# Kernel optimization log

Hardware: AMD Instinct MI355X
Metric: run time of the kernel (lower is better)

Reference implementation:

```python
import jax, jax.numpy as jnp
import numpy as np
from jax import lax

PRE_NMS_TOPN = 2000
POST_NMS_TOPN = 1000
NMS_THRESH = 0.7
MIN_BOX_SIZE = 4.0
BBOX_XFORM_CLIP = 4.135  # log(1000/16), standard clamp on dw/dh


def setup_inputs() -> dict:
    key = jax.random.key(0)
    k1, k2, k3, k4 = jax.random.split(key, 4)
    B, N = 8, 250000
    H, W = 800, 1333
    rpn_bbox_pred = jax.random.normal(k1, (B, N, 4), jnp.float32) * 0.5
    objectness = jax.random.normal(k2, (B, N), jnp.float32)
    # realistic anchors: centers inside image, sizes in [16, 256]
    ctr = jax.random.uniform(k3, (N, 2), jnp.float32) * jnp.array([W, H], jnp.float32)
    wh = jax.random.uniform(k4, (N, 2), jnp.float32) * 240.0 + 16.0
    anchors = jnp.concatenate([ctr - 0.5 * wh, ctr + 0.5 * wh], axis=-1)
    return {"rpn_bbox_pred": rpn_bbox_pred, "objectness": objectness,
            "anchors": anchors, "height": H, "width": W}


def _decode_clip(anchors, deltas, height, width):
    # anchors (1,N,4) broadcast against deltas (B,N,4); boxes are x1,y1,x2,y2
    aw = anchors[..., 2] - anchors[..., 0]
    ah = anchors[..., 3] - anchors[..., 1]
    ax = anchors[..., 0] + 0.5 * aw
    ay = anchors[..., 1] + 0.5 * ah
    dx, dy = deltas[..., 0], deltas[..., 1]
    dw = jnp.minimum(deltas[..., 2], BBOX_XFORM_CLIP)
    dh = jnp.minimum(deltas[..., 3], BBOX_XFORM_CLIP)
    px = dx * aw + ax
    py = dy * ah + ay
    pw = jnp.exp(dw) * aw
    ph = jnp.exp(dh) * ah
    x1 = jnp.clip(px - 0.5 * pw, 0.0, float(width))
    y1 = jnp.clip(py - 0.5 * ph, 0.0, float(height))
    x2 = jnp.clip(px + 0.5 * pw, 0.0, float(width))
    y2 = jnp.clip(py + 0.5 * ph, 0.0, float(height))
    return jnp.stack([x1, y1, x2, y2], axis=-1)


def _pairwise_iou(boxes):
    # boxes (K,4) -> iou (K,K)
    x1, y1, x2, y2 = boxes[:, 0], boxes[:, 1], boxes[:, 2], boxes[:, 3]
    area = (x2 - x1) * (y2 - y1)
    iw = jnp.maximum(jnp.minimum(x2[:, None], x2[None, :]) - jnp.maximum(x1[:, None], x1[None, :]), 0.0)
    ih = jnp.maximum(jnp.minimum(y2[:, None], y2[None, :]) - jnp.maximum(y1[:, None], y1[None, :]), 0.0)
    inter = iw * ih
    return inter / (area[:, None] + area[None, :] - inter + 1e-9)


def _nms_keep(boxes, valid):
    # sequential greedy NMS over score-sorted boxes (K,4); returns keep mask (K,)
    iou = lax.stop_gradient(_pairwise_iou(boxes))
    idxs = jnp.arange(PRE_NMS_TOPN)
    def body(i, keep):
        sup = (iou[i] > NMS_THRESH) & keep[i] & (idxs > i)
        return keep & (~sup)
    return lax.fori_loop(0, PRE_NMS_TOPN, body, valid)


def _per_image(boxes, scores):
    # boxes (N,4), scores (N,)
    ws = boxes[:, 2] - boxes[:, 0]
    hs = boxes[:, 3] - boxes[:, 1]
    size_ok = (ws >= MIN_BOX_SIZE) & (hs >= MIN_BOX_SIZE)
    masked = jnp.where(size_ok, scores, -jnp.inf)
    top_s, order = lax.top_k(masked, PRE_NMS_TOPN)   # descending sort + pre-NMS topN
    top_boxes = boxes[order]                          # (PRE,4)
    valid = top_s > -jnp.inf                          # boxes surviving size filter
    keep = _nms_keep(top_boxes, valid)
    # take first POST_NMS_TOPN kept boxes in score order (fixed-shape padding)
    sel = jnp.sort(jnp.where(keep, jnp.arange(PRE_NMS_TOPN), PRE_NMS_TOPN))[:POST_NMS_TOPN]
    out_valid = sel < PRE_NMS_TOPN
    sel_c = jnp.minimum(sel, PRE_NMS_TOPN - 1)
    out = jnp.where(out_valid[:, None], top_boxes[sel_c], 0.0)
    return out, out_valid


def reference(rpn_bbox_pred, objectness, anchors, height, width):
    proposals = _decode_clip(anchors[None], rpn_bbox_pred, height, width)  # (B,N,4)
    out, valid = jax.vmap(_per_image)(proposals, objectness)
    # padded equivalent of the ragged per-image list: (B,POST,4) boxes + (B,POST) validity
    return out, valid
```

## Files before the change

### kernel.cpp

```cpp
#include <hip/hip_runtime.h>
#include <hip/hip_bf16.h>

#define NBUCK 8192
#define P1B   64
#define CAP   4096
#define TOPN  2000
#define NP2   2048
#define OUTN  1000
#define NST   64
#define NSLOT 8
#define SLOTW 2048

typedef unsigned int u32x4 __attribute__((ext_vector_type(4)));
typedef __attribute__((address_space(1))) const unsigned GUP;
typedef __attribute__((address_space(3))) unsigned LUP;

__device__ __forceinline__ float4 decode_box(const float4 a, const float4 d, float W, float H) {
    float aw = a.z - a.x;
    float ah = a.w - a.y;
    float ax = a.x + 0.5f * aw;
    float ay = a.y + 0.5f * ah;
    float dw = fminf(d.z, 4.135f);
    float dh = fminf(d.w, 4.135f);
    float px = d.x * aw + ax;
    float py = d.y * ah + ay;
    float pw = expf(dw) * aw;
    float ph = expf(dh) * ah;
    float4 r;
    r.x = fminf(fmaxf(px - 0.5f * pw, 0.0f), W);
    r.y = fminf(fmaxf(py - 0.5f * ph, 0.0f), H);
    r.z = fminf(fmaxf(px + 0.5f * pw, 0.0f), W);
    r.w = fminf(fmaxf(py + 0.5f * ph, 0.0f), H);
    return r;
}

__device__ __forceinline__ unsigned score_key(const float4 a, const float4 d, float W, float H, float s) {
    float4 b = decode_box(a, d, W, H);
    bool ok = ((b.z - b.x) >= 4.0f) && ((b.w - b.y) >= 4.0f);
    float ms = ok ? s : -INFINITY;
    unsigned u = __float_as_uint(ms);
    return (u & 0x80000000u) ? ~u : (u | 0x80000000u);
}

__global__ void __launch_bounds__(1024) k_pass1(const float* __restrict__ pred,
        const float* __restrict__ obj, const float* __restrict__ anch,
        const int* __restrict__ Hp, const int* __restrict__ Wp,
        unsigned* __restrict__ keys, unsigned short* __restrict__ bhist,
        unsigned* __restrict__ cnt, unsigned* __restrict__ remInit, int N) {
    __shared__ unsigned h[NBUCK];
    int t = threadIdx.x;
    int b = blockIdx.y, g = blockIdx.x;
    if (g == 0 && t < 64) { if (t == 0) cnt[b * 64] = 0; remInit[b * 64 + t] = 0; }
    for (int i = t; i < NBUCK; i += 1024) h[i] = 0;
    __syncthreads();
    int chunk = (N + P1B - 1) / P1B;
    int base = g * chunk;
    int end = base + chunk; if (end > N) end = N;
    float W = (float)*Wp, H = (float)*Hp;
    for (int n = base + t; n < end; n += 1024) {
        float4 a = ((const float4*)anch)[n];
        float4 d = ((const float4*)pred)[(size_t)b * N + n];
        float s = obj[(size_t)b * N + n];
        unsigned key = score_key(a, d, W, H, s);
        keys[(size_t)b * N + n] = key;
        atomicAdd(&h[key >> 19], 1u);
    }
    __syncthreads();
    unsigned short* bh = bhist + ((size_t)(b * P1B + g)) * NBUCK;
    int i0 = t * 8;
    uint4 pk;
    pk.x = (h[i0 + 0] & 0xFFFFu) | (h[i0 + 1] << 16);
    pk.y = (h[i0 + 2] & 0xFFFFu) | (h[i0 + 3] << 16);
    pk.z = (h[i0 + 4] & 0xFFFFu) | (h[i0 + 5] << 16);
    pk.w = (h[i0 + 6] & 0xFFFFu) | (h[i0 + 7] << 16);
    *(uint4*)(bh + i0) = pk;
}

__global__ void __launch_bounds__(1024) k_scanA(const unsigned short* __restrict__ bhist,
                                                unsigned* __restrict__ hist32) {
    int b = blockIdx.y, p = blockIdx.x, t = threadIdx.x;
    int bkt = p * 1024 + t;
    const unsigned short* src = bhist + (size_t)b * P1B * NBUCK + bkt;
    unsigned acc = 0;
    #pragma unroll 8
    for (int g = 0; g < P1B; g++) acc += src[(size_t)g * NBUCK];
    hist32[b * NBUCK + bkt] = acc;
}

__global__ void k_scanB(const unsigned* __restrict__ hist32, unsigned* __restrict__ Lb) {
    __shared__ unsigned h[NBUCK];
    __shared__ unsigned csum[256];
    __shared__ unsigned suf[256];
    __shared__ int tcS;
    __shared__ unsigned befS;
    int b = blockIdx.x, t = threadIdx.x;
    const unsigned* src = hist32 + (size_t)b * NBUCK;
    for (int i = t * 4; i < NBUCK; i += 1024) {
        uint4 v = *(const uint4*)(src + i);
        h[i] = v.x; h[i + 1] = v.y; h[i + 2] = v.z; h[i + 3] = v.w;
    }
    if (t == 0) tcS = -1;
    __syncthreads();
    unsigned s = 0;
    for (int j = 0; j < 32; j++) s += h[t * 32 + j];
    csum[t] = s; suf[t] = s;
    __syncthreads();
    for (int d = 1; d < 256; d <<= 1) {
        unsigned v = (t + d < 256) ? suf[t + d] : 0;
        __syncthreads();
        suf[t] += v;
        __syncthreads();
    }
    if (suf[t] >= (unsigned)TOPN && (t == 255 || suf[t + 1] < (unsigned)TOPN)) {
        tcS = t; befS = (t == 255) ? 0u : suf[t + 1];
    }
    __syncthreads();
    if (t == 0) {
        unsigned L = 0;
        int tc = tcS;
        if (tc >= 0) {
            unsigned r = befS;
            for (int bkt = tc * 32 + 31;; bkt--) {
                r += h[bkt];
                if (r >= (unsigned)TOPN || bkt == tc * 32) { L = (unsigned)bkt; break; }
            }
        }
        Lb[b] = L;
    }
}

__global__ void k_collect(const unsigned* __restrict__ keys, const unsigned* __restrict__ Lb,
                          unsigned* __restrict__ count, unsigned long long* __restrict__ cand,
                          int N) {
    __shared__ unsigned lk[1024], ln[1024];
    __shared__ unsigned lcnt, lbase;
    int b = blockIdx.y, t = threadIdx.x;
    if (t == 0) lcnt = 0;
    __syncthreads();
    unsigned L = Lb[b];
    const unsigned* kb = keys + (size_t)b * N;
    int e = blockIdx.x * 256 + t;
    int n0 = e * 4;
    if (n0 + 3 < N) {
        uint4 kv = ((const uint4*)kb)[e];
        if ((kv.x >> 19) >= L) { unsigned p = atomicAdd(&lcnt, 1u); lk[p] = kv.x; ln[p] = n0; }
        if ((kv.y >> 19) >= L) { unsigned p = atomicAdd(&lcnt, 1u); lk[p] = kv.y; ln[p] = n0 + 1; }
        if ((kv.z >> 19) >= L) { unsigned p = atomicAdd(&lcnt, 1u); lk[p] = kv.z; ln[p] = n0 + 2; }
        if ((kv.w >> 19) >= L) { unsigned p = atomicAdd(&lcnt, 1u); lk[p] = kv.w; ln[p] = n0 + 3; }
    } else {
        for (int j = 0; j < 4; j++) {
            int n = n0 + j;
            if (n < N) {
                unsigned k = kb[n];
                if ((k >> 19) >= L) { unsigned p = atomicAdd(&lcnt, 1u); lk[p] = k; ln[p] = n; }
            }
        }
    }
    __syncthreads();
    if (t == 0) lbase = atomicAdd(&count[b * 64], lcnt);
    __syncthreads();
    unsigned c = lcnt, bs = lbase;
    for (unsigned i = t; i < c; i += 256) {
        unsigned pos = bs + i;
        if (pos < CAP) cand[(size_t)b * CAP + pos] =
            ((unsigned long long)lk[i] << 32) | (unsigned)(~ln[i]);
    }
}

#define REGX(e, p, d, lo)  ((lo) == (d) ? ((e) >= (p) ? (e) : (p)) : ((e) >= (p) ? (p) : (e)))

__global__ void __launch_bounds__(256) k_sort1(unsigned long long* __restrict__ cand,
        const unsigned* __restrict__ count) {
    __shared__ unsigned long long s[512];
    int b = blockIdx.x >> 3, g = blockIdx.x & 7;
    int t = threadIdx.x;
    unsigned cnt = count[b * 64]; if (cnt > CAP) cnt = CAP;
    unsigned long long* cb = cand + (size_t)b * CAP + g * 512;
    if ((unsigned)(g * 512) >= cnt) {
        cb[t] = 0ULL; cb[t + 256] = 0ULL;
        return;
    }
    int g0 = g * 512 + t, g1 = g * 512 + t + 256;
    unsigned long long e0 = (g0 < (int)cnt) ? cb[t] : 0ULL;
    unsigned long long e1 = (g1 < (int)cnt) ? cb[t + 256] : 0ULL;

    #pragma unroll
    for (int k = 2; k <= 64; k <<= 1) {
        bool d0 = ((g0 & k) == 0);
        bool d1 = ((g1 & k) == 0);
        #pragma unroll
        for (int j = k >> 1; j >= 1; j >>= 1) {
            bool lo = ((t & j) == 0);
            unsigned long long p0 = __shfl_xor(e0, j, 64);
            unsigned long long p1 = __shfl_xor(e1, j, 64);
            e0 = REGX(e0, p0, d0, lo);
            e1 = REGX(e1, p1, d1, lo);
        }
    }
    for (int k = 128; k <= 512; k <<= 1) {
        s[t] = e0; s[t + 256] = e1;
        __syncthreads();
        for (int j = k >> 1; j >= 64; j >>= 1) {
            int i = ((t & ~(j - 1)) << 1) | (t & (j - 1));
            int l = i + j;
            bool desc = (((g * 512 + i) & k) == 0);
            unsigned long long x = s[i], y = s[l];
            if (desc ? (x < y) : (x > y)) { s[i] = y; s[l] = x; }
            __syncthreads();
        }
        e0 = s[t]; e1 = s[t + 256];
        bool d0 = ((g0 & k) == 0);
        bool d1 = ((g1 & k) == 0);
        #pragma unroll
        for (int j = 32; j >= 1; j >>= 1) {
            bool lo = ((t & j) == 0);
            unsigned long long p0 = __shfl_xor(e0, j, 64);
            unsigned long long p1 = __shfl_xor(e1, j, 64);
            e0 = REGX(e0, p0, d0, lo);
            e1 = REGX(e1, p1, d1, lo);
        }
    }
    cb[t] = e0; cb[t + 256] = e1;
}

__global__ void __launch_bounds__(1024) k_sort2(const unsigned long long* __restrict__ cand,
        const unsigned* __restrict__ count,
        const float* __restrict__ pred, const float* __restrict__ anch,
        const int* __restrict__ Hp, const int* __restrict__ Wp,
        float4* __restrict__ topbox, unsigned* __restrict__ remInit, int N) {
    __shared__ unsigned long long s[CAP];
    int b = blockIdx.x, t = threadIdx.x;
    const unsigned long long* cb = cand + (size_t)b * CAP;
    unsigned cnt = count[b * 64]; if (cnt > CAP) cnt = CAP;
    unsigned long long e0, e1;
    if (cnt <= 2048) {
        e0 = cb[t]; e1 = cb[t + 1024];
        for (int k = 1024; k <= 2048; k <<= 1) {
            s[t] = e0; s[t + 1024] = e1;
            __syncthreads();
            for (int j = k >> 1; j >= 64; j >>= 1) {
                int i = ((t & ~(j - 1)) << 1) | (t & (j - 1));
                int l = i + j;
                bool desc = ((i & k) == 0);
                unsigned long long x = s[i], y = s[l];
                if (desc ? (x < y) : (x > y)) { s[i] = y; s[l] = x; }
                __syncthreads();
            }
            e0 = s[t]; e1 = s[t + 1024];
            bool d0 = ((t & k) == 0);
            bool d1 = (((t + 1024) & k) == 0);
            #pragma unroll
            for (int j = 32; j >= 1; j >>= 1) {
                bool lo = ((t & j) == 0);
                unsigned long long p0 = __shfl_xor(e0, j, 64);
                unsigned long long p1 = __shfl_xor(e1, j, 64);
                e0 = REGX(e0, p0, d0, lo);
                e1 = REGX(e1, p1, d1, lo);
            }
        }
    } else {
        unsigned long long f0 = cb[t], f1 = cb[t + 1024], f2 = cb[t + 2048], f3 = cb[t + 3072];
        for (int k = 1024; k <= 4096; k <<= 1) {
            s[t] = f0; s[t + 1024] = f1; s[t + 2048] = f2; s[t + 3072] = f3;
            __syncthreads();
            for (int j = k >> 1; j >= 64; j >>= 1) {
                #pragma unroll
                for (int cc = 0; cc < 2; cc++) {
                    int c = t + cc * 1024;
                    int i = ((c & ~(j - 1)) << 1) | (c & (j - 1));
                    int l = i + j;
                    bool desc = ((i & k) == 0);
                    unsigned long long x = s[i], y = s[l];
                    if (desc ? (x < y) : (x > y)) { s[i] = y; s[l] = x; }
                }
                __syncthreads();
            }
            f0 = s[t]; f1 = s[t + 1024]; f2 = s[t + 2048]; f3 = s[t + 3072];
            bool d0 = ((t & k) == 0);
            bool d1 = (((t + 1024) & k) == 0);
            bool d2 = (((t + 2048) & k) == 0);
            bool d3 = (((t + 3072) & k) == 0);
            #pragma unroll
            for (int j = 32; j >= 1; j >>= 1) {
                bool lo = ((t & j) == 0);
                unsigned long long p0 = __shfl_xor(f0, j, 64);
                unsigned long long p1 = __shfl_xor(f1, j, 64);
                unsigned long long p2 = __shfl_xor(f2, j, 64);
                unsigned long long p3 = __shfl_xor(f3, j, 64);
                f0 = REGX(f0, p0, d0, lo);
                f1 = REGX(f1, p1, d1, lo);
                f2 = REGX(f2, p2, d2, lo);
                f3 = REGX(f3, p3, d3, lo);
            }
        }
        e0 = f0; e1 = f1;
    }
    float W = (float)*Wp, H = (float)*Hp;
    #pragma unroll
    for (int m = 0; m < 2; m++) {
        unsigned long long v = m ? e1 : e0;
        int r = t + m * 1024;
        unsigned key = (unsigned)(v >> 32);
        bool valid = key > 0x007FFFFFu;
        float4 outb = {0.f, 0.f, 0.f, 0.f};
        if (valid) {
            unsigned idx = ~((unsigned)v);
            float4 a = ((const float4*)anch)[idx];
            float4 d = ((const float4*)pred)[(size_t)b * N + idx];
            outb = decode_box(a, d, W, H);
        }
        topbox[(size_t)b * NP2 + r] = outb;
        if (r < TOPN && !valid) atomicOr(&remInit[b * 64 + (r >> 5)], 1u << (r & 31));
    }
}

__global__ void __launch_bounds__(256) k_mask(const float4* __restrict__ topbox,
                                              unsigned* __restrict__ maskT) {
    const double MID = 23488103.0 / 33554432.0;
    __shared__ float4 bx[NP2];
    __shared__ float ar[NP2];
    int b = blockIdx.y, cp = blockIdx.x;
    int t = threadIdx.x;
    int j0 = cp * 32;
    for (int i = j0 + t; i < NP2; i += 256) {
        float4 v = topbox[(size_t)b * NP2 + i];
        bx[i] = v;
        ar[i] = (v.z - v.x) * (v.w - v.y);
    }
    __syncthreads();
    int r = t & 31;
    int wg = t >> 5;
    #pragma unroll
    for (int half = 0; half < 2; half++) {
        int c = half ? (63 - cp) : cp;
        int i = c * 32 + r;
        float4 bi = bx[i];
        float areai = ar[i];
        unsigned* outc = maskT + ((size_t)(b * NST + c)) * SLOTW;
        for (int w = wg; w < c; w += 8) outc[w * 32 + r] = 0u;
        for (int w = c + wg; w < 64; w += 8) {
            unsigned bits = 0;
            int jbase = w * 32;
            #pragma unroll
            for (int jj = 0; jj < 32; jj++) {
                int j = jbase + jj;
                float4 bj = bx[j];
                float iw = fmaxf(fminf(bi.z, bj.z) - fmaxf(bi.x, bj.x), 0.0f);
                float ih = fmaxf(fminf(bi.w, bj.w) - fmaxf(bi.y, bj.y), 0.0f);
                float inter = iw * ih;
                float denom = areai + ar[j] - inter + 1e-9f;
                if ((double)inter >= MID * (double)denom) bits |= (1u << jj);
            }
            if (w == c) bits &= ~((2u << r) - 1u);
            outc[w * 32 + r] = bits;
        }
    }
}

__global__ void __launch_bounds__(512) k_nms(const unsigned* __restrict__ maskT,
        const unsigned* __restrict__ remInit, const float4* __restrict__ topbox,
        float* __restrict__ out, int B) {
    __shared__ __align__(16) unsigned smbuf[NSLOT * SLOTW];
    __shared__ int ready[NST];
    __shared__ int consumed;
    __shared__ int stop;
    int b = blockIdx.x;
    int t = threadIdx.x;
    const unsigned* m = maskT + (size_t)b * NST * SLOTW;

    float4* ob = (float4*)out + (size_t)b * OUTN;
    for (int i = t; i < OUTN; i += 512) ob[i] = make_float4(0.f, 0.f, 0.f, 0.f);
    float* vout = out + (size_t)B * (OUTN * 4) + (size_t)b * OUTN;
    for (int i = t; i < OUTN; i += 512) vout[i] = 0.0f;

    if (t < NST) ready[t] = 0;
    if (t == 0) { consumed = 0; stop = 0; }
    __syncthreads();

    unsigned removed = 0xFFFFFFFFu;

    if (t >= 64) {
        int w = t >> 6;
        int lam = t & 63;
        int base = ((lam >> 3) << 5) + ((((lam & 7) ^ ((lam >> 3) & 7))) << 2);
        #pragma unroll 1
        for (int s = w - 1; s < NST; s += 7) {
            if (__hip_atomic_load(&stop, __ATOMIC_RELAXED, __HIP_MEMORY_SCOPE_WORKGROUP)) break;
            while (__hip_atomic_load(&consumed, __ATOMIC_ACQUIRE,
                   __HIP_MEMORY_SCOPE_WORKGROUP) < s - (NSLOT - 1))
                __builtin_amdgcn_s_sleep(2);
            const unsigned* gs = m + (size_t)s * SLOTW + base;
            unsigned* sl = smbuf + (s & (NSLOT - 1)) * SLOTW;
            #pragma unroll
            for (int i = 0; i < 8; i++)
                __builtin_amdgcn_global_load_lds((GUP*)(gs + i * 256),
                                                 (LUP*)(sl + i * 256), 16, 0, 0);
            asm volatile("s_waitcnt vmcnt(0)" ::: "memory");
            if (lam == 0) __hip_atomic_store(&ready[s], 1, __ATOMIC_RELEASE,
                                             __HIP_MEMORY_SCOPE_WORKGROUP);
        }
    } else {
        removed = remInit[b * 64 + t];
        if (t == 62) removed |= 0xFFFF0000u;
        if (t == 63) removed = 0xFFFFFFFFu;
        int e = t & 7;
        int keptRun = 0;
        #pragma unroll 1
        for (int s = 0; s < NST; s++) {
            while (!__hip_atomic_load(&ready[s], __ATOMIC_ACQUIRE,
                   __HIP_MEMORY_SCOPE_WORKGROUP))
                __builtin_amdgcn_s_sleep(2);
            const u32x4* sq = (const u32x4*)(smbuf + (s & (NSLOT - 1)) * SLOTW) + t * 8;
            unsigned R[32];
            #pragma unroll
            for (int k = 0; k < 8; k++) *(u32x4*)&R[k << 2] = sq[k ^ e];
            __builtin_amdgcn_sched_group_barrier(0x100, 8, 0);
            unsigned alive = ~__builtin_amdgcn_readlane(removed, s);
            unsigned Is[32];
            #pragma unroll
            for (int q = 0; q < 32; q++) Is[q] = __builtin_amdgcn_readlane(R[q], s);
            #pragma unroll
            for (int q = 0; q < 32; q++) alive &= ~(((alive >> q) & 1u) ? Is[q] : 0u);
            unsigned a0 = 0, a1 = 0, a2 = 0, a3 = 0;
            #pragma unroll
            for (int q = 0; q < 32; q += 4) {
                a0 |= ((alive >> q) & 1u)       ? R[q]     : 0u;
                a1 |= ((alive >> (q + 1)) & 1u) ? R[q + 1] : 0u;
                a2 |= ((alive >> (q + 2)) & 1u) ? R[q + 2] : 0u;
                a3 |= ((alive >> (q + 3)) & 1u) ? R[q + 3] : 0u;
            }
            removed |= (a0 | a1) | (a2 | a3);
            keptRun += __popc(~__builtin_amdgcn_readlane(removed, s));
            if (keptRun >= OUTN) {
                if (t == 0) {
                    __hip_atomic_store(&stop, 1, __ATOMIC_RELAXED, __HIP_MEMORY_SCOPE_WORKGROUP);
                    __hip_atomic_store(&consumed, NST, __ATOMIC_RELEASE, __HIP_MEMORY_SCOPE_WORKGROUP);
                }
                break;
            }
            if (t == 0) __hip_atomic_store(&consumed, s + 1, __ATOMIC_RELEASE,
                                           __HIP_MEMORY_SCOPE_WORKGROUP);
        }
        unsigned keep = ~removed;
        int cnt = __popc(keep);
        int ex = cnt;
        for (int off = 1; off < 64; off <<= 1) {
            int v = __shfl_up(ex, off, 64);
            if (t >= off) ex += v;
        }
        ex -= cnt;
        int pos = ex;
        for (int j = 0; j < 32; j++) {
            if ((keep >> j) & 1u) {
                if (pos < OUTN) {
                    float4 bxv = topbox[(size_t)b * NP2 + t * 32 + j];
                    ob[pos] = bxv;
                    vout[pos] = 1.0f;
                }
                pos++;
            }
        }
    }
}

extern "C" void kernel_launch(void* const* d_in, const int* in_sizes, int n_in,
                              void* d_out, int out_size, void* d_ws, size_t ws_size,
                              hipStream_t stream) {
    const float* pred = (const float*)d_in[0];
    const float* obj  = (const float*)d_in[1];
    const float* anch = (const float*)d_in[2];
    const int* Hp = (const int*)d_in[3];
    const int* Wp = (const int*)d_in[4];
    int N = in_sizes[2] / 4;
    int B = in_sizes[1] / N;

    char* ws = (char*)d_ws;
    size_t off = 0;
    auto take = [&](size_t bytes) { void* p = ws + off; off = (off + bytes + 255) & ~(size_t)255; return p; };

    size_t regA_bytes = (size_t)B * N * 4;
    size_t mask_bytes = (size_t)B * NST * SLOTW * 4;
    char* regA = (char*)take(regA_bytes > mask_bytes ? regA_bytes : mask_bytes);
    unsigned* keys  = (unsigned*)regA;
    unsigned* maskT = (unsigned*)regA;
    unsigned short* bhist    = (unsigned short*)take((size_t)B * P1B * NBUCK * 2);
    unsigned* hist32         = (unsigned*)take((size_t)B * NBUCK * 4);
    unsigned long long* cand = (unsigned long long*)take((size_t)B * CAP * 8);
    float4* topbox           = (float4*)take((size_t)B * NP2 * 16);
    unsigned* cnt            = (unsigned*)take((size_t)B * 64 * 4);
    unsigned* Lb             = (unsigned*)take((size_t)B * 64 * 4);
    unsigned* remInit        = (unsigned*)take((size_t)B * 64 * 4);

    k_pass1  <<<dim3(P1B, B), 1024, 0, stream>>>(pred, obj, anch, Hp, Wp, keys, bhist, cnt, remInit, N);
    k_scanA  <<<dim3(8, B), 1024, 0, stream>>>(bhist, hist32);
    k_scanB  <<<B, 256, 0, stream>>>(hist32, Lb);
    k_collect<<<dim3((N + 1023) / 1024, B), 256, 0, stream>>>(keys, Lb, cnt, cand, N);
    k_sort1  <<<B * 8, 256, 0, stream>>>(cand, cnt);
    k_sort2  <<<B, 1024, 0, stream>>>(cand, cnt, pred, anch, Hp, Wp, topbox, remInit, N);
    k_mask   <<<dim3(32, B), 256, 0, stream>>>(topbox, maskT);
    k_nms    <<<B, 512, 0, stream>>>(maskT, remInit, topbox, (float*)d_out, B);
}
```

Baseline: 117.3 us.

## Merge scan and sort kernel pairs using last-block-done atomic counters

Folds k_scanA/k_scanB into one kernel and k_sort1/k_sort2 into one kernel. In each, the block that finishes last for an image, detected with an agent-scope atomic counter, carries on with the follow-up step, so two kernel launches and their launch gaps go away. In exchange, the sort kernel now launches 1024 threads with 32KB of shared memory even though only 256 threads work in the first phase, which lowers occupancy. The final per-image stage is also serialized behind the slowest block.

```diff
diff --git a/kernel.cpp b/kernel.cpp
--- a/kernel.cpp
+++ b/kernel.cpp
@@ -46,11 +46,15 @@
         const float* __restrict__ obj, const float* __restrict__ anch,
         const int* __restrict__ Hp, const int* __restrict__ Wp,
         unsigned* __restrict__ keys, unsigned short* __restrict__ bhist,
-        unsigned* __restrict__ cnt, unsigned* __restrict__ remInit, int N) {
+        unsigned* __restrict__ cnt, unsigned* __restrict__ remInit,
+        unsigned* __restrict__ done, int N) {
     __shared__ unsigned h[NBUCK];
     int t = threadIdx.x;
     int b = blockIdx.y, g = blockIdx.x;
-    if (g == 0 && t < 64) { if (t == 0) cnt[b * 64] = 0; remInit[b * 64 + t] = 0; }
+    if (g == 0 && t < 64) {
+        if (t == 0) { cnt[b * 64] = 0; done[b] = 0; }
+        remInit[b * 64 + t] = 0;
+    }
     for (int i = t; i < NBUCK; i += 1024) h[i] = 0;
     __syncthreads();
     int chunk = (N + P1B - 1) / P1B;
@@ -76,8 +80,15 @@
     *(uint4*)(bh + i0) = pk;
 }
 
-__global__ void __launch_bounds__(1024) k_scanA(const unsigned short* __restrict__ bhist,
-                                                unsigned* __restrict__ hist32) {
+__global__ void __launch_bounds__(1024) k_scan(const unsigned short* __restrict__ bhist,
+        unsigned* __restrict__ hist32, unsigned* __restrict__ done,
+        unsigned* __restrict__ Lb, unsigned* __restrict__ sdone) {
+    __shared__ unsigned h[NBUCK];
+    __shared__ unsigned csum[256];
+    __shared__ unsigned suf[256];
+    __shared__ int tcS;
+    __shared__ unsigned befS;
+    __shared__ int lastFlag;
     int b = blockIdx.y, p = blockIdx.x, t = threadIdx.x;
     int bkt = p * 1024 + t;
     const unsigned short* src = bhist + (size_t)b * P1B * NBUCK + bkt;
@@ -85,33 +96,35 @@
     #pragma unroll 8
     for (int g = 0; g < P1B; g++) acc += src[(size_t)g * NBUCK];
     hist32[b * NBUCK + bkt] = acc;
-}
-
-__global__ void k_scanB(const unsigned* __restrict__ hist32, unsigned* __restrict__ Lb) {
-    __shared__ unsigned h[NBUCK];
-    __shared__ unsigned csum[256];
-    __shared__ unsigned suf[256];
-    __shared__ int tcS;
-    __shared__ unsigned befS;
-    int b = blockIdx.x, t = threadIdx.x;
-    const unsigned* src = hist32 + (size_t)b * NBUCK;
-    for (int i = t * 4; i < NBUCK; i += 1024) {
-        uint4 v = *(const uint4*)(src + i);
-        h[i] = v.x; h[i + 1] = v.y; h[i + 2] = v.z; h[i + 3] = v.w;
-    }
+    __threadfence();
+    __syncthreads();
+    if (t == 0) {
+        unsigned d = __hip_atomic_fetch_add(&done[b], 1u, __ATOMIC_ACQ_REL,
+                                            __HIP_MEMORY_SCOPE_AGENT);
+        lastFlag = (d == 7);
+        if (d == 7) sdone[b] = 0;
+    }
+    __syncthreads();
+    if (!lastFlag) return;
+    __threadfence();
+    for (int i = t; i < NBUCK; i += 1024)
+        h[i] = __hip_atomic_load(&hist32[b * NBUCK + i], __ATOMIC_RELAXED,
+                                 __HIP_MEMORY_SCOPE_AGENT);
     if (t == 0) tcS = -1;
     __syncthreads();
-    unsigned s = 0;
-    for (int j = 0; j < 32; j++) s += h[t * 32 + j];
-    csum[t] = s; suf[t] = s;
+    if (t < 256) {
+        unsigned s = 0;
+        for (int j = 0; j < 32; j++) s += h[t * 32 + j];
+        csum[t] = s; suf[t] = s;
+    }
     __syncthreads();
     for (int d = 1; d < 256; d <<= 1) {
-        unsigned v = (t + d < 256) ? suf[t + d] : 0;
+        unsigned v = (t < 256 && t + d < 256) ? suf[t + d] : 0;
         __syncthreads();
-        suf[t] += v;
+        if (t < 256) suf[t] += v;
         __syncthreads();
     }
-    if (suf[t] >= (unsigned)TOPN && (t == 255 || suf[t + 1] < (unsigned)TOPN)) {
+    if (t < 256 && suf[t] >= (unsigned)TOPN && (t == 255 || suf[t + 1] < (unsigned)TOPN)) {
         tcS = t; befS = (t == 255) ? 0u : suf[t + 1];
     }
     __syncthreads();
@@ -120,9 +133,9 @@
         int tc = tcS;
         if (tc >= 0) {
             unsigned r = befS;
-            for (int bkt = tc * 32 + 31;; bkt--) {
-                r += h[bkt];
-                if (r >= (unsigned)TOPN || bkt == tc * 32) { L = (unsigned)bkt; break; }
+            for (int bkt2 = tc * 32 + 31;; bkt2--) {
+                r += h[bkt2];
+                if (r >= (unsigned)TOPN || bkt2 == tc * 32) { L = (unsigned)bkt2; break; }
             }
         }
         Lb[b] = L;
@@ -169,72 +182,85 @@
 
 #define REGX(e, p, d, lo)  ((lo) == (d) ? ((e) >= (p) ? (e) : (p)) : ((e) >= (p) ? (p) : (e)))
 
-__global__ void __launch_bounds__(256) k_sort1(unsigned long long* __restrict__ cand,
-        const unsigned* __restrict__ count) {
-    __shared__ unsigned long long s[512];
+__global__ void __launch_bounds__(1024) k_sort(unsigned long long* __restrict__ cand,
+        const unsigned* __restrict__ count, unsigned* __restrict__ sdone,
+        const float* __restrict__ pred, const float* __restrict__ anch,
+        const int* __restrict__ Hp, const int* __restrict__ Wp,
+        float4* __restrict__ topbox, unsigned* __restrict__ remInit, int N) {
+    __shared__ unsigned long long s[CAP];
+    __shared__ int lastFlag;
     int b = blockIdx.x >> 3, g = blockIdx.x & 7;
     int t = threadIdx.x;
     unsigned cnt = count[b * 64]; if (cnt > CAP) cnt = CAP;
     unsigned long long* cb = cand + (size_t)b * CAP + g * 512;
+
     if ((unsigned)(g * 512) >= cnt) {
-        cb[t] = 0ULL; cb[t + 256] = 0ULL;
-        return;
-    }
-    int g0 = g * 512 + t, g1 = g * 512 + t + 256;
-    unsigned long long e0 = (g0 < (int)cnt) ? cb[t] : 0ULL;
-    unsigned long long e1 = (g1 < (int)cnt) ? cb[t + 256] : 0ULL;
-
-    #pragma unroll
-    for (int k = 2; k <= 64; k <<= 1) {
-        bool d0 = ((g0 & k) == 0);
-        bool d1 = ((g1 & k) == 0);
-        #pragma unroll
-        for (int j = k >> 1; j >= 1; j >>= 1) {
-            bool lo = ((t & j) == 0);
-            unsigned long long p0 = __shfl_xor(e0, j, 64);
-            unsigned long long p1 = __shfl_xor(e1, j, 64);
-            e0 = REGX(e0, p0, d0, lo);
-            e1 = REGX(e1, p1, d1, lo);
-        }
-    }
-    for (int k = 128; k <= 512; k <<= 1) {
-        s[t] = e0; s[t + 256] = e1;
-        __syncthreads();
-        for (int j = k >> 1; j >= 64; j >>= 1) {
-            int i = ((t & ~(j - 1)) << 1) | (t & (j - 1));
-            int l = i + j;
-            bool desc = (((g * 512 + i) & k) == 0);
-            unsigned long long x = s[i], y = s[l];
-            if (desc ? (x < y) : (x > y)) { s[i] = y; s[l] = x; }
+        if (t < 256) { cb[t] = 0ULL; cb[t + 256] = 0ULL; }
+    } else {
+        int g0 = g * 512 + t, g1 = g * 512 + t + 256;
+        unsigned long long e0 = 0, e1 = 0;
+        if (t < 256) {
+            e0 = (g0 < (int)cnt) ? cb[t] : 0ULL;
+            e1 = (g1 < (int)cnt) ? cb[t + 256] : 0ULL;
+            #pragma unroll
+            for (int k = 2; k <= 64; k <<= 1) {
+                bool d0 = ((g0 & k) == 0);
+                bool d1 = ((g1 & k) == 0);
+                #pragma unroll
+                for (int j = k >> 1; j >= 1; j >>= 1) {
+                    bool lo = ((t & j) == 0);
+                    unsigned long long p0 = __shfl_xor(e0, j, 64);
+                    unsigned long long p1 = __shfl_xor(e1, j, 64);
+                    e0 = REGX(e0, p0, d0, lo);
+                    e1 = REGX(e1, p1, d1, lo);
+                }
+            }
+        }
+        for (int k = 128; k <= 512; k <<= 1) {
+            if (t < 256) { s[t] = e0; s[t + 256] = e1; }
             __syncthreads();
-        }
-        e0 = s[t]; e1 = s[t + 256];
-        bool d0 = ((g0 & k) == 0);
-        bool d1 = ((g1 & k) == 0);
-        #pragma unroll
-        for (int j = 32; j >= 1; j >>= 1) {
-            bool lo = ((t & j) == 0);
-            unsigned long long p0 = __shfl_xor(e0, j, 64);
-            unsigned long long p1 = __shfl_xor(e1, j, 64);
-            e0 = REGX(e0, p0, d0, lo);
-            e1 = REGX(e1, p1, d1, lo);
-        }
-    }
-    cb[t] = e0; cb[t + 256] = e1;
-}
-
-__global__ void __launch_bounds__(1024) k_sort2(const unsigned long long* __restrict__ cand,
-        const unsigned* __restrict__ count,
-        const float* __restrict__ pred, const float* __restrict__ anch,
-        const int* __restrict__ Hp, const int* __restrict__ Wp,
-        float4* __restrict__ topbox, unsigned* __restrict__ remInit, int N) {
-    __shared__ unsigned long long s[CAP];
-    int b = blockIdx.x, t = threadIdx.x;
-    const unsigned long long* cb = cand + (size_t)b * CAP;
-    unsigned cnt = count[b * 64]; if (cnt > CAP) cnt = CAP;
+            for (int j = k >> 1; j >= 64; j >>= 1) {
+                if (t < 256) {
+                    int i = ((t & ~(j - 1)) << 1) | (t & (j - 1));
+                    int l = i + j;
+                    bool desc = (((g * 512 + i) & k) == 0);
+                    unsigned long long x = s[i], y = s[l];
+                    if (desc ? (x < y) : (x > y)) { s[i] = y; s[l] = x; }
+                }
+                __syncthreads();
+            }
+            if (t < 256) {
+                e0 = s[t]; e1 = s[t + 256];
+                bool d0 = ((g0 & k) == 0);
+                bool d1 = ((g1 & k) == 0);
+                #pragma unroll
+                for (int j = 32; j >= 1; j >>= 1) {
+                    bool lo = ((t & j) == 0);
+                    unsigned long long p0 = __shfl_xor(e0, j, 64);
+                    unsigned long long p1 = __shfl_xor(e1, j, 64);
+                    e0 = REGX(e0, p0, d0, lo);
+                    e1 = REGX(e1, p1, d1, lo);
+                }
+            }
+        }
+        if (t < 256) { cb[t] = e0; cb[t + 256] = e1; }
+    }
+
+    __threadfence();
+    __syncthreads();
+    if (t == 0) {
+        unsigned d = __hip_atomic_fetch_add(&sdone[b], 1u, __ATOMIC_ACQ_REL,
+                                            __HIP_MEMORY_SCOPE_AGENT);
+        lastFlag = (d == 7);
+    }
+    __syncthreads();
+    if (!lastFlag) return;
+    __threadfence();
+
+    const unsigned long long* cbb = cand + (size_t)b * CAP;
     unsigned long long e0, e1;
     if (cnt <= 2048) {
-        e0 = cb[t]; e1 = cb[t + 1024];
+        e0 = cbb[t]; e1 = cbb[t + 1024];
         for (int k = 1024; k <= 2048; k <<= 1) {
             s[t] = e0; s[t + 1024] = e1;
             __syncthreads();
@@ -259,7 +285,7 @@
             }
         }
     } else {
-        unsigned long long f0 = cb[t], f1 = cb[t + 1024], f2 = cb[t + 2048], f3 = cb[t + 3072];
+        unsigned long long f0 = cbb[t], f1 = cbb[t + 1024], f2 = cbb[t + 2048], f3 = cbb[t + 3072];
         for (int k = 1024; k <= 4096; k <<= 1) {
             s[t] = f0; s[t + 1024] = f1; s[t + 2048] = f2; s[t + 3072] = f3;
             __syncthreads();
@@ -490,13 +516,13 @@
     unsigned* cnt            = (unsigned*)take((size_t)B * 64 * 4);
     unsigned* Lb             = (unsigned*)take((size_t)B * 64 * 4);
     unsigned* remInit        = (unsigned*)take((size_t)B * 64 * 4);
-
-    k_pass1  <<<dim3(P1B, B), 1024, 0, stream>>>(pred, obj, anch, Hp, Wp, keys, bhist, cnt, remInit, N);
-    k_scanA  <<<dim3(8, B), 1024, 0, stream>>>(bhist, hist32);
-    k_scanB  <<<B, 256, 0, stream>>>(hist32, Lb);
+    unsigned* done           = (unsigned*)take((size_t)B * 4);
+    unsigned* sdone          = (unsigned*)take((size_t)B * 4);
+
+    k_pass1  <<<dim3(P1B, B), 1024, 0, stream>>>(pred, obj, anch, Hp, Wp, keys, bhist, cnt, remInit, done, N);
+    k_scan   <<<dim3(8, B), 1024, 0, stream>>>(bhist, hist32, done, Lb, sdone);
     k_collect<<<dim3((N + 1023) / 1024, B), 256, 0, stream>>>(keys, Lb, cnt, cand, N);
-    k_sort1  <<<B * 8, 256, 0, stream>>>(cand, cnt);
-    k_sort2  <<<B, 1024, 0, stream>>>(cand, cnt, pred, anch, Hp, Wp, topbox, remInit, N);
+    k_sort   <<<B * 8, 1024, 0, stream>>>(cand, cnt, sdone, pred, anch, Hp, Wp, topbox, remInit, N);
     k_mask   <<<dim3(32, B), 256, 0, stream>>>(topbox, maskT);
     k_nms    <<<B, 512, 0, stream>>>(maskT, remInit, topbox, (float*)d_out, B);
 }
```

Measured after the change: 174.9 us. 49.0% more time.
